# Kernel tuning notes

Measured on AMD Instinct MI355X. Metric: run time of the kernel, lower is better.

The kernel has to match this reference:

```python
import jax, jax.numpy as jnp
import numpy as np

KH, KW = 3, 3  # kernel_size
PH, PW = (KH - 1) // 2, (KW - 1) // 2  # zero padding, matches _compute_zero_padding


def setup_inputs() -> dict:
    key = jax.random.key(0)
    x = jax.random.normal(key, (16, 3, 512, 512), dtype=jnp.float32)
    return {"x": x}


def reference(x):
    B, C, H, W = x.shape
    # zero-pad spatially, same as F.conv2d(padding=(PH, PW))
    xp = jnp.pad(x, ((0, 0), (0, 0), (PH, PH), (PW, PW)))
    # unfold KHxKW sliding windows: loop over fixed 9 kernel offsets (not a data dim)
    patches = jnp.stack(
        [xp[:, :, i : i + H, j : j + W] for i in range(KH) for j in range(KW)],
        axis=2,
    )  # (B, C, KH*KW, H, W)
    # odd window size (9): jnp.median == torch.median (lower median irrelevant)
    return jnp.median(patches, axis=2)
```

## Files before the change

### kernel.cpp

```cpp
#include <hip/hip_runtime.h>


#define MIN3(a, b, c) fminf(fminf(a, b), c)
#define MAX3(a, b, c) fmaxf(fmaxf(a, b), c)
#define MED3(a, b, c) __builtin_amdgcn_fmed3f(a, b, c)

constexpr int H = 512, W = 512;
constexpr int RPS = 8;

__device__ __forceinline__ void load6(const float* __restrict__ rowp, int x0,
                                      bool valid, float v[6]) {
    if (valid) {
        const float4 q = *reinterpret_cast<const float4*>(rowp + x0);
        v[1] = q.x; v[2] = q.y; v[3] = q.z; v[4] = q.w;
        v[0] = (x0 > 0)     ? rowp[x0 - 1] : 0.0f;
        v[5] = (x0 + 4 < W) ? rowp[x0 + 4] : 0.0f;
    } else {
        v[0] = v[1] = v[2] = 0.0f;
        v[3] = v[4] = v[5] = 0.0f;
    }
}

__global__ __launch_bounds__(256) void median3x3_kernel(
    const float* __restrict__ in, float* __restrict__ out) {
    const int tid = threadIdx.x;
    const int lane = tid & 127;
    const int strip = tid >> 7;
    const int x0 = lane << 2;

    const int rg0 = blockIdx.x * (2 * RPS) + strip * RPS;
    const int plane = rg0 >> 9;
    const int y0 = rg0 & (H - 1);

    const float* base = in + (size_t)plane * H * W;
    float* obase = out + (size_t)plane * H * W;

    float c0[6], c1[6], c2[6];
    load6(base + (size_t)(y0 - 1) * W, x0, y0 > 0, c0);
    load6(base + (size_t)y0 * W, x0, true, c1);

#pragma unroll
    for (int r = 0; r < RPS; ++r) {
        const int yn = y0 + r + 1;
        load6(base + (size_t)yn * W, x0, yn < H, c2);

        float lo[6], mi[6], hi[6];
#pragma unroll
        for (int j = 0; j < 6; ++j) {
            lo[j] = MIN3(c0[j], c1[j], c2[j]);
            mi[j] = MED3(c0[j], c1[j], c2[j]);
            hi[j] = MAX3(c0[j], c1[j], c2[j]);
        }

        float4 o;
        float res[4];
#pragma unroll
        for (int k = 0; k < 4; ++k) {
            const float a = MAX3(lo[k], lo[k + 1], lo[k + 2]);
            const float b = MED3(mi[k], mi[k + 1], mi[k + 2]);
            const float c = MIN3(hi[k], hi[k + 1], hi[k + 2]);
            res[k] = MED3(a, b, c);
        }
        o.x = res[0]; o.y = res[1]; o.z = res[2]; o.w = res[3];
        *reinterpret_cast<float4*>(obase + (size_t)(y0 + r) * W + x0) = o;

#pragma unroll
        for (int j = 0; j < 6; ++j) { c0[j] = c1[j]; c1[j] = c2[j]; }
    }
}

extern "C" void kernel_launch(void* const* d_in, const int* in_sizes, int n_in,
                              void* d_out, int out_size, void* d_ws, size_t ws_size,
                              hipStream_t stream) {
    const float* x = (const float*)d_in[0];
    float* out = (float*)d_out;
    const int nblocks = (16 * 3 * H) / (2 * RPS);
    median3x3_kernel<<<nblocks, 256, 0, stream>>>(x, out);
}
```

Before: 25.84 us.

## Use wavefront shuffles for halo pixels and remap blocks to single-wave half rows

Halo columns now come from neighbouring lanes through __shfl_up/__shfl_down instead of extra scalar global loads. Only the edge lanes of each 64-wide wave still read from memory. Blocks shrink to one 64-thread wavefront that covers half a row-strip, and the block index is swizzled so consecutive blocks are spread across eight interleaved groups, likely to balance work across XCDs or channels. This cuts redundant load instructions but quadruples the number of small blocks, adds cross-lane ops, and makes each wave's row segment shorter.

```diff
diff --git a/kernel.cpp b/kernel.cpp
--- a/kernel.cpp
+++ b/kernel.cpp
@@ -7,28 +7,34 @@
 
 constexpr int H = 512, W = 512;
 constexpr int RPS = 8;
+constexpr int NBLOCKS = (16 * 3 * H / RPS) * 2;
 
-__device__ __forceinline__ void load6(const float* __restrict__ rowp, int x0,
-                                      bool valid, float v[6]) {
+__device__ __forceinline__ void load_row(const float* __restrict__ rowp, int x0,
+                                         int lane, bool valid, float v[6]) {
     if (valid) {
         const float4 q = *reinterpret_cast<const float4*>(rowp + x0);
-        v[1] = q.x; v[2] = q.y; v[3] = q.z; v[4] = q.w;
-        v[0] = (x0 > 0)     ? rowp[x0 - 1] : 0.0f;
-        v[5] = (x0 + 4 < W) ? rowp[x0 + 4] : 0.0f;
+        float lft = __shfl_up(q.w, 1);
+        float rgt = __shfl_down(q.x, 1);
+        if (lane == 0)  lft = (x0 > 0)     ? rowp[x0 - 1] : 0.0f;
+        if (lane == 63) rgt = (x0 + 4 < W) ? rowp[x0 + 4] : 0.0f;
+        v[0] = lft; v[1] = q.x; v[2] = q.y; v[3] = q.z; v[4] = q.w; v[5] = rgt;
     } else {
         v[0] = v[1] = v[2] = 0.0f;
         v[3] = v[4] = v[5] = 0.0f;
     }
 }
 
-__global__ __launch_bounds__(256) void median3x3_kernel(
+__global__ __launch_bounds__(64) void median3x3_kernel(
     const float* __restrict__ in, float* __restrict__ out) {
-    const int tid = threadIdx.x;
-    const int lane = tid & 127;
-    const int strip = tid >> 7;
-    const int x0 = lane << 2;
+    const int braw = blockIdx.x;
+    const int bid = (braw & 7) * (NBLOCKS / 8) + (braw >> 3);
 
-    const int rg0 = blockIdx.x * (2 * RPS) + strip * RPS;
+    const int half = bid & 1;
+    const int strip = bid >> 1;
+    const int lane = threadIdx.x;
+    const int x0 = half * 256 + (lane << 2);
+
+    const int rg0 = strip * RPS;
     const int plane = rg0 >> 9;
     const int y0 = rg0 & (H - 1);
 
@@ -36,13 +42,13 @@
     float* obase = out + (size_t)plane * H * W;
 
     float c0[6], c1[6], c2[6];
-    load6(base + (size_t)(y0 - 1) * W, x0, y0 > 0, c0);
-    load6(base + (size_t)y0 * W, x0, true, c1);
+    load_row(base + (size_t)(y0 - 1) * W, x0, lane, y0 > 0, c0);
+    load_row(base + (size_t)y0 * W, x0, lane, true, c1);
 
 #pragma unroll
     for (int r = 0; r < RPS; ++r) {
         const int yn = y0 + r + 1;
-        load6(base + (size_t)yn * W, x0, yn < H, c2);
+        load_row(base + (size_t)yn * W, x0, lane, yn < H, c2);
 
         float lo[6], mi[6], hi[6];
 #pragma unroll
@@ -52,7 +58,6 @@
             hi[j] = MAX3(c0[j], c1[j], c2[j]);
         }
 
-        float4 o;
         float res[4];
 #pragma unroll
         for (int k = 0; k < 4; ++k) {
@@ -61,6 +66,7 @@
             const float c = MIN3(hi[k], hi[k + 1], hi[k + 2]);
             res[k] = MED3(a, b, c);
         }
+        float4 o;
         o.x = res[0]; o.y = res[1]; o.z = res[2]; o.w = res[3];
         *reinterpret_cast<float4*>(obase + (size_t)(y0 + r) * W + x0) = o;
 
@@ -74,6 +80,5 @@
                               hipStream_t stream) {
     const float* x = (const float*)d_in[0];
     float* out = (float*)d_out;
-    const int nblocks = (16 * 3 * H) / (2 * RPS);
-    median3x3_kernel<<<nblocks, 256, 0, stream>>>(x, out);
+    median3x3_kernel<<<NBLOCKS, 64, 0, stream>>>(x, out);
 }
```

Result: no change. 25.55 us (-1.1%).
